# Kernel tuning notes

Measured on AMD Instinct MI355X. Metric: run time of the kernel, lower is better.

Reference implementation:

```python
import jax, jax.numpy as jnp
import numpy as np

N = 100000  # nodes

def gcn_layer(x, W, b, src, dst, norm):
    # x: [N, Fin] -> [N, Fout]; symmetric-normalized aggregation (PyG GCNConv)
    h = x @ W                                   # linear first (no bias yet)
    msg = h[src] * norm[:, None]                # gather + edge-wise scale
    out = jax.ops.segment_sum(msg, dst, num_segments=N)  # scatter-add to targets
    return out + b

def _prep_edges(edge_index):
    # add self loops
    loops = jnp.arange(N, dtype=edge_index.dtype)
    src = jnp.concatenate([edge_index[0], loops])
    dst = jnp.concatenate([edge_index[1], loops])
    # deg computed on target nodes with unit edge weights
    deg = jax.ops.segment_sum(jnp.ones_like(dst, dtype=jnp.float32), dst, num_segments=N)
    dinv = jnp.where(deg > 0, jax.lax.rsqrt(deg), 0.0)
    norm = dinv[src] * dinv[dst]
    return src, dst, norm

def setup_inputs() -> dict:
    key = jax.random.key(0)
    ks = jax.random.split(key, 8)
    F_in, H1, H2, C = 512, 256, 64, 10
    E = 3200000
    x = jax.random.normal(ks[0], (N, F_in), dtype=jnp.float32)
    edge_index = jax.random.randint(ks[1], (2, E), 0, N, dtype=jnp.int64)
    def glorot(k, fan_in, fan_out):
        s = jnp.sqrt(6.0 / (fan_in + fan_out))
        return jax.random.uniform(k, (fan_in, fan_out), jnp.float32, -s, s)
    return {
        "x": x,
        "edge_index": edge_index,
        "W1": glorot(ks[2], F_in, H1), "b1": jnp.zeros((H1,), jnp.float32),
        "W2": glorot(ks[3], H1, H2),   "b2": jnp.zeros((H2,), jnp.float32),
        "W3": glorot(ks[4], H2, C),    "b3": jnp.zeros((C,), jnp.float32),
    }

def reference(x, edge_index, W1, b1, W2, b2, W3, b3):
    src, dst, norm = _prep_edges(edge_index)
    h = jax.nn.relu(gcn_layer(x, W1, b1, src, dst, norm))
    h = jax.nn.relu(gcn_layer(h, W2, b2, src, dst, norm))
    h = gcn_layer(h, W3, b3, src, dst, norm)
    return jax.nn.log_softmax(h, axis=1)
```

## Files before the change

kernel.cpp:

```cpp
#include <hip/hip_runtime.h>
#include <math.h>

#define NNODES 100000
#define NEDGES 3200000
#define NB 391
#define PB 512
#define CHUNK 6250

typedef __attribute__((ext_vector_type(4))) float f32x4;
typedef __attribute__((ext_vector_type(2))) float f32x2;
typedef __attribute__((ext_vector_type(8))) short bf16x8;

__device__ __forceinline__ float bf2f(ushort u) {
    union { unsigned u; float f; } v; v.u = ((unsigned)u) << 16; return v.f;
}
__device__ __forceinline__ ushort f2bf(float f) {
    union { float f; unsigned u; } v; v.f = f;
    unsigned r = v.u + 0x7FFFu + ((v.u >> 16) & 1u);
    return (ushort)(r >> 16);
}

#if __has_builtin(__builtin_amdgcn_cvt_pk_fp8_f32) && __has_builtin(__builtin_amdgcn_cvt_pk_f32_fp8)
#define FP8_HW 1
#else
#define FP8_HW 0
#endif

__device__ __forceinline__ unsigned fp8enc_sw(float f) {
    union { float f; unsigned u; } v; v.f = f;
    unsigned sign = v.u >> 31;
    float a = fabsf(f);
    if (a >= 448.0f) return (sign << 7) | 0x7E;
    if (a < 0.0009765625f) return sign << 7;
    unsigned u = v.u & 0x7FFFFFFFu;
    u += 0x7FFFFu + ((u >> 20) & 1u);
    int e2 = (int)(u >> 23) - 127;
    if (e2 < -6) {
        int m = (int)(a * 512.0f + 0.5f); if (m > 7) m = 7;
        return (sign << 7) | (unsigned)m;
    }
    if (e2 > 8) return (sign << 7) | 0x7E;
    unsigned mant = (u >> 20) & 7u;
    return (sign << 7) | ((unsigned)(e2 + 7) << 3) | mant;
}
__device__ __forceinline__ float fp8dec_sw(unsigned b) {
    unsigned s = b >> 7, e = (b >> 3) & 0xF, m = b & 7;
    float v;
    if (e == 0) v = (float)m * 0.001953125f;
    else { union { unsigned u; float f; } x; x.u = ((e + 120u) << 23) | (m << 20); v = x.f; }
    return s ? -v : v;
}

__device__ __forceinline__ unsigned char f2fp8(float f) {
#if FP8_HW
    return (unsigned char)(__builtin_amdgcn_cvt_pk_fp8_f32(f, 0.f, 0, false) & 0xFF);
#else
    return (unsigned char)fp8enc_sw(f);
#endif
}
__device__ __forceinline__ void fp8x4_acc(unsigned w, float& ax, float& ay, float& az, float& aw) {
#if FP8_HW
    f32x2 lo = __builtin_amdgcn_cvt_pk_f32_fp8((int)w, false);
    f32x2 hi = __builtin_amdgcn_cvt_pk_f32_fp8((int)w, true);
    ax += lo[0]; ay += lo[1]; az += hi[0]; aw += hi[1];
#else
    ax += fp8dec_sw(w & 0xFF); ay += fp8dec_sw((w >> 8) & 0xFF);
    az += fp8dec_sw((w >> 16) & 0xFF); aw += fp8dec_sw(w >> 24);
#endif
}

__global__ void bucket_hist(const int* __restrict__ dst, int e, int* __restrict__ hist) {
    __shared__ int h[NB];
    const int b = blockIdx.x, t = threadIdx.x;
    for (int j = t; j < NB; j += 256) h[j] = 0;
    __syncthreads();
    const int lo = b * CHUNK;
    int hi = lo + CHUNK; if (hi > e) hi = e;
    for (int i = lo + t; i < hi; i += 256)
        atomicAdd(&h[dst[i] >> 8], 1);
    __syncthreads();
    for (int j = t; j < NB; j += 256) hist[b * NB + j] = h[j];
}

__global__ void scan_buckets(int* __restrict__ hist, int* __restrict__ btotal) {
    __shared__ int s[256];
    const int j = blockIdx.x, t = threadIdx.x;
    int v0 = hist[(2 * t) * NB + j];
    int v1 = hist[(2 * t + 1) * NB + j];
    int p = v0 + v1;
    s[t] = p;
    __syncthreads();
    for (int off = 1; off < 256; off <<= 1) {
        int u = (t >= off) ? s[t - off] : 0;
        __syncthreads();
        s[t] += u;
        __syncthreads();
    }
    int excl = s[t] - p;
    hist[(2 * t) * NB + j] = excl;
    hist[(2 * t + 1) * NB + j] = excl + v0;
    if (t == 255) btotal[j] = s[255];
}

__global__ void scan_btotal(const int* __restrict__ btotal, int* __restrict__ bstart, int e) {
    __shared__ int s[512];
    const int t = threadIdx.x;
    int v = (t < NB) ? btotal[t] : 0;
    s[t] = v;
    __syncthreads();
    for (int off = 1; off < 512; off <<= 1) {
        int u = (t >= off) ? s[t - off] : 0;
        __syncthreads();
        s[t] += u;
        __syncthreads();
    }
    if (t < NB) bstart[t] = s[t] - v;
    if (t == 0) bstart[NB] = e;
}

__global__ void bucket_scatter(const int* __restrict__ src, const int* __restrict__ dst, int e,
                               const int* __restrict__ hist, const int* __restrict__ bstart,
                               unsigned* __restrict__ bucketed) {
    __shared__ int off[NB];
    const int b = blockIdx.x, t = threadIdx.x;
    for (int j = t; j < NB; j += 256) off[j] = bstart[j] + hist[b * NB + j];
    __syncthreads();
    const int lo = b * CHUNK;
    int hi = lo + CHUNK; if (hi > e) hi = e;
    for (int i = lo + t; i < hi; i += 256) {
        int d = dst[i];
        int j = d >> 8;
        int p = atomicAdd(&off[j], 1);
        bucketed[p] = (unsigned)src[i] | ((unsigned)(d & 255) << 24);
    }
}

__global__ void bucket_finalize(const unsigned* __restrict__ bucketed, const int* __restrict__ bstart,
                                float* __restrict__ dinv, int* __restrict__ rowptr,
                                int* __restrict__ esrc, int n, int e) {
    __shared__ int h[256];
    __shared__ int s[256];
    __shared__ int rp[256];
    const int j = blockIdx.x, t = threadIdx.x;
    h[t] = 0;
    __syncthreads();
    const int lo = bstart[j], hi = bstart[j + 1];
    for (int i = lo + t; i < hi; i += 256)
        atomicAdd(&h[bucketed[i] >> 24], 1);
    __syncthreads();
    const int c = h[t] + 1;
    s[t] = c;
    __syncthreads();
    for (int off = 1; off < 256; off <<= 1) {
        int u = (t >= off) ? s[t - off] : 0;
        __syncthreads();
        s[t] += u;
        __syncthreads();
    }
    const int excl = s[t] - c;
    const int base = j << 8;
    const int node = base + t;
    const int myrp = bstart[j] + base + excl;
    rp[t] = myrp;
    if (node < n) {
        dinv[node] = rsqrtf((float)c);
        rowptr[node] = myrp;
        esrc[myrp] = node;
    }
    if (j == 0 && t == 0) rowptr[n] = e + n;
    h[t] = 0;
    __syncthreads();
    for (int i = lo + t; i < hi; i += 256) {
        unsigned ed = bucketed[i];
        int l = ed >> 24;
        int off = atomicAdd(&h[l], 1);
        esrc[rp[l] + 1 + off] = (int)(ed & 0xFFFFFFu);
    }
}

__global__ void conv_bf16(const float* __restrict__ x, ushort* __restrict__ xb, long n4) {
    long i = (long)blockIdx.x * blockDim.x + threadIdx.x;
    long stride = (long)gridDim.x * blockDim.x;
    for (; i < n4; i += stride) {
        float4 v = ((const float4*)x)[i];
        ushort4 o;
        o.x = f2bf(v.x); o.y = f2bf(v.y); o.z = f2bf(v.z); o.w = f2bf(v.w);
        ((ushort4*)xb)[i] = o;
    }
}

__global__ void conv_wt(const float* __restrict__ W, ushort* __restrict__ Wt,
                        int K, int N, int Npad) {
    int idx = blockIdx.x * blockDim.x + threadIdx.x;
    if (idx >= Npad * K) return;
    int n = idx / K, k = idx % K;
    Wt[idx] = (n < N) ? f2bf(W[(size_t)k * N + n]) : (ushort)0;
}

template <int BM, int BN, int BK, int WM, int WN, int OUTK>
__launch_bounds__(WM* WN * 64)
__global__ void gemm_bf16(const ushort* __restrict__ A, const ushort* __restrict__ Bt,
                          const float* __restrict__ dinv, void* __restrict__ Cout,
                          int M, int N, int K) {
    constexpr int NT = WM * WN * 64;
    __shared__ __align__(16) ushort As[BM][BK];
    __shared__ __align__(16) ushort Bs[BN][BK];
    const int tid = threadIdx.x;
    const int wid = tid >> 6, lane = tid & 63;
    const int wr = wid / WN, wc = wid % WN;
    constexpr int TM = BM / WM, TN = BN / WN;
    constexpr int FM = TM / 16, FN = TN / 16;
    const int m0 = blockIdx.y * BM, n0 = blockIdx.x * BN;
    const int ln = lane & 15, ks = (lane >> 4) * 8;

    f32x4 acc[FM][FN] = {};

    constexpr int ACH = BM * BK / 8;
    constexpr int BCH = BN * BK / 8;
    constexpr int CPR = BK / 8;

    for (int k0 = 0; k0 < K; k0 += BK) {
        #pragma unroll
        for (int it = 0; it < (ACH + NT - 1) / NT; ++it) {
            int c = it * NT + tid;
            if ((ACH % NT == 0) || (c < ACH)) {
                int row = c / CPR, ch = c % CPR;
                int gm = m0 + row; if (gm >= M) gm = M - 1;
                const ushort* gp = &A[(size_t)gm * K + k0 + ch * 8];
                __builtin_amdgcn_global_load_lds(
                    (const __attribute__((address_space(1))) void*)gp,
                    (__attribute__((address_space(3))) void*)((char*)&As[0][0] + c * 16),
                    16, 0, 0);
            }
        }
        #pragma unroll
        for (int it = 0; it < (BCH + NT - 1) / NT; ++it) {
            int c = it * NT + tid;
            if ((BCH % NT == 0) || (c < BCH)) {
                int row = c / CPR, ch = c % CPR;
                const ushort* gp = &Bt[(size_t)(n0 + row) * K + k0 + ch * 8];
                __builtin_amdgcn_global_load_lds(
                    (const __attribute__((address_space(1))) void*)gp,
                    (__attribute__((address_space(3))) void*)((char*)&Bs[0][0] + c * 16),
                    16, 0, 0);
            }
        }
        __syncthreads();

        bf16x8 af[FM], bfr[FN];
        #pragma unroll
        for (int mi = 0; mi < FM; ++mi)
            af[mi] = *(const bf16x8*)&As[wr * TM + mi * 16 + ln][ks];
        #pragma unroll
        for (int nj = 0; nj < FN; ++nj)
            bfr[nj] = *(const bf16x8*)&Bs[wc * TN + nj * 16 + ln][ks];
        #pragma unroll
        for (int mi = 0; mi < FM; ++mi)
            #pragma unroll
            for (int nj = 0; nj < FN; ++nj)
                acc[mi][nj] = __builtin_amdgcn_mfma_f32_16x16x32_bf16(af[mi], bfr[nj], acc[mi][nj], 0, 0, 0);
        __syncthreads();
    }

    const int rbase = (lane >> 4) * 4;
    #pragma unroll
    for (int mi = 0; mi < FM; ++mi) {
        #pragma unroll
        for (int r = 0; r < 4; ++r) {
            int gm = m0 + wr * TM + mi * 16 + rbase + r;
            if (gm >= M) continue;
            float d = dinv[gm];
            #pragma unroll
            for (int nj = 0; nj < FN; ++nj) {
                int gn = n0 + wc * TN + nj * 16 + ln;
                float v = acc[mi][nj][r] * d;
                if (OUTK == 1)      ((float*)Cout)[(size_t)gm * N + gn] = v;
                else if (OUTK == 0) ((ushort*)Cout)[(size_t)gm * N + gn] = f2bf(v);
                else                ((unsigned char*)Cout)[(size_t)gm * N + gn] = f2fp8(v);
            }
        }
    }
}

__global__ void agg1_fp8(const unsigned* __restrict__ h, const int* __restrict__ rowptr,
                         const int* __restrict__ esrc, const float* __restrict__ dinv,
                         const float* __restrict__ bias, ushort* __restrict__ out, int n) {
    const int wid = threadIdx.x >> 6, lane = threadIdx.x & 63;
    const int i = blockIdx.x * 4 + wid;
    if (i >= n) return;
    const int lo = rowptr[i], hi = rowptr[i + 1];
    float ax = 0.f, ay = 0.f, az = 0.f, aw = 0.f;
    int e = lo;
    for (; e + 7 < hi; e += 8) {
        int s[8];
        unsigned w[8];
        #pragma unroll
        for (int q = 0; q < 8; ++q) s[q] = esrc[e + q];
        #pragma unroll
        for (int q = 0; q < 8; ++q) w[q] = h[(size_t)s[q] * 64 + lane];
        #pragma unroll
        for (int q = 0; q < 8; ++q) fp8x4_acc(w[q], ax, ay, az, aw);
    }
    for (; e < hi; ++e)
        fp8x4_acc(h[(size_t)esrc[e] * 64 + lane], ax, ay, az, aw);

    float d = dinv[i];
    const int f0 = lane * 4;
    float4 b = *(const float4*)&bias[f0];
    ushort4 o;
    o.x = f2bf(fmaxf(ax * d + b.x, 0.f));
    o.y = f2bf(fmaxf(ay * d + b.y, 0.f));
    o.z = f2bf(fmaxf(az * d + b.z, 0.f));
    o.w = f2bf(fmaxf(aw * d + b.w, 0.f));
    *(ushort4*)&out[(size_t)i * 256 + f0] = o;
}

__global__ void agg2_fp8(const unsigned* __restrict__ h, const int* __restrict__ rowptr,
                         const int* __restrict__ esrc, const float* __restrict__ dinv,
                         const float* __restrict__ bias, ushort* __restrict__ out, int n) {
    const int g = threadIdx.x >> 4, j = threadIdx.x & 15;
    const int i = blockIdx.x * 16 + g;
    if (i >= n) return;
    const int lo = rowptr[i], hi = rowptr[i + 1];
    float ax = 0.f, ay = 0.f, az = 0.f, aw = 0.f;
    int e = lo;
    for (; e + 3 < hi; e += 4) {
        int s0 = esrc[e], s1 = esrc[e + 1], s2 = esrc[e + 2], s3 = esrc[e + 3];
        unsigned w0 = h[(size_t)s0 * 16 + j];
        unsigned w1 = h[(size_t)s1 * 16 + j];
        unsigned w2 = h[(size_t)s2 * 16 + j];
        unsigned w3 = h[(size_t)s3 * 16 + j];
        fp8x4_acc(w0, ax, ay, az, aw);
        fp8x4_acc(w1, ax, ay, az, aw);
        fp8x4_acc(w2, ax, ay, az, aw);
        fp8x4_acc(w3, ax, ay, az, aw);
    }
    for (; e < hi; ++e)
        fp8x4_acc(h[(size_t)esrc[e] * 16 + j], ax, ay, az, aw);

    float d = dinv[i];
    const int f0 = j * 4;
    float4 b = *(const float4*)&bias[f0];
    ushort4 o;
    o.x = f2bf(fmaxf(ax * d + b.x, 0.f));
    o.y = f2bf(fmaxf(ay * d + b.y, 0.f));
    o.z = f2bf(fmaxf(az * d + b.z, 0.f));
    o.w = f2bf(fmaxf(aw * d + b.w, 0.f));
    *(ushort4*)&out[(size_t)i * 64 + f0] = o;
}

__global__ void agg3_logsoftmax(const ushort* __restrict__ h3, const int* __restrict__ rowptr,
                                const int* __restrict__ esrc, const float* __restrict__ dinv,
                                const float* __restrict__ bias, float* __restrict__ out, int n) {
    const int g = threadIdx.x >> 3, j = threadIdx.x & 7;
    const int i = blockIdx.x * 32 + g;
    if (i >= n) return;
    const int lo = rowptr[i], hi = rowptr[i + 1];
    float a0 = 0.f, a1 = 0.f;
    int e = lo;
    for (; e + 3 < hi; e += 4) {
        int s0 = esrc[e], s1 = esrc[e + 1], s2 = esrc[e + 2], s3 = esrc[e + 3];
        unsigned w0 = *(const unsigned*)&h3[(size_t)s0 * 16 + 2 * j];
        unsigned w1 = *(const unsigned*)&h3[(size_t)s1 * 16 + 2 * j];
        unsigned w2 = *(const unsigned*)&h3[(size_t)s2 * 16 + 2 * j];
        unsigned w3 = *(const unsigned*)&h3[(size_t)s3 * 16 + 2 * j];
        a0 += bf2f((ushort)(w0 & 0xFFFF)) + bf2f((ushort)(w1 & 0xFFFF))
            + bf2f((ushort)(w2 & 0xFFFF)) + bf2f((ushort)(w3 & 0xFFFF));
        a1 += bf2f((ushort)(w0 >> 16)) + bf2f((ushort)(w1 >> 16))
            + bf2f((ushort)(w2 >> 16)) + bf2f((ushort)(w3 >> 16));
    }
    for (; e < hi; ++e) {
        unsigned w = *(const unsigned*)&h3[(size_t)esrc[e] * 16 + 2 * j];
        a0 += bf2f((ushort)(w & 0xFFFF));
        a1 += bf2f((ushort)(w >> 16));
    }
    const int f0 = 2 * j;
    float d = dinv[i];
    float v0 = (f0 < 10) ? (a0 * d + bias[f0]) : -INFINITY;
    float v1 = (f0 + 1 < 10) ? (a1 * d + bias[f0 + 1]) : -INFINITY;
    float m = fmaxf(v0, v1);
    #pragma unroll
    for (int off = 1; off < 8; off <<= 1) m = fmaxf(m, __shfl_xor(m, off, 8));
    float ex = ((f0 < 10) ? expf(v0 - m) : 0.f) + ((f0 + 1 < 10) ? expf(v1 - m) : 0.f);
    #pragma unroll
    for (int off = 1; off < 8; off <<= 1) ex += __shfl_xor(ex, off, 8);
    float ls = logf(ex);
    if (f0 < 10)     out[(size_t)i * 10 + f0] = v0 - m - ls;
    if (f0 + 1 < 10) out[(size_t)i * 10 + f0 + 1] = v1 - m - ls;
}

extern "C" void kernel_launch(void* const* d_in, const int* in_sizes, int n_in,
                              void* d_out, int out_size, void* d_ws, size_t ws_size,
                              hipStream_t stream) {
    const int N = NNODES, E = NEDGES;
    const float* x  = (const float*)d_in[0];
    const int*   ei = (const int*)d_in[1];
    const float* W1 = (const float*)d_in[2];
    const float* b1 = (const float*)d_in[3];
    const float* W2 = (const float*)d_in[4];
    const float* b2 = (const float*)d_in[5];
    const float* W3 = (const float*)d_in[6];
    const float* b3 = (const float*)d_in[7];
    float* out = (float*)d_out;
    const int* src = ei;
    const int* dst = ei + E;

    char* ws = (char*)d_ws;
    size_t off = 0;
    auto alloc = [&](size_t bytes) -> void* {
        void* p = ws + off;
        off = (off + bytes + 255) & ~(size_t)255;
        return p;
    };
    float* dinv   = (float*)alloc((size_t)N * 4);
    int*   rowptr = (int*)alloc((size_t)(N + 1) * 4);
    int*   btotal = (int*)alloc((size_t)NB * 4);
    int*   bstart = (int*)alloc((size_t)(NB + 1) * 4);
    int*   esrc   = (int*)alloc((size_t)(E + N) * 4);
    ushort* xb    = (ushort*)alloc((size_t)N * 512 * 2);
    ushort* W1t   = (ushort*)alloc((size_t)256 * 512 * 2);
    ushort* W2t   = (ushort*)alloc((size_t)64 * 256 * 2);
    ushort* W3t   = (ushort*)alloc((size_t)16 * 64 * 2);
    ushort* buf1  = (ushort*)alloc((size_t)N * 256 * 2);
    ushort* buf2  = (ushort*)alloc((size_t)N * 256 * 2);
    int*   hist   = (int*)buf1;
    unsigned* bucketed = (unsigned*)buf2;
    unsigned char* h1fp8 = (unsigned char*)buf1;
    unsigned char* h2fp8 = (unsigned char*)buf1;
    ushort* h3b   = (ushort*)xb;

    const int T = 256;
    bucket_hist<<<PB, T, 0, stream>>>(dst, E, hist);
    scan_buckets<<<NB, T, 0, stream>>>(hist, btotal);
    scan_btotal<<<1, 512, 0, stream>>>(btotal, bstart, E);
    bucket_scatter<<<PB, T, 0, stream>>>(src, dst, E, hist, bstart, bucketed);
    bucket_finalize<<<NB, T, 0, stream>>>(bucketed, bstart, dinv, rowptr, esrc, N, E);

    conv_bf16<<<2048, T, 0, stream>>>(x, xb, (long)N * 512 / 4);
    conv_wt<<<(256 * 512 + T - 1) / T, T, 0, stream>>>(W1, W1t, 512, 256, 256);
    conv_wt<<<(64 * 256 + T - 1) / T, T, 0, stream>>>(W2, W2t, 256, 64, 64);
    conv_wt<<<(16 * 64 + T - 1) / T, T, 0, stream>>>(W3, W3t, 64, 10, 16);

    const int MB = (N + 127) / 128;

    gemm_bf16<128, 128, 32, 2, 2, 2><<<dim3(2, MB), 256, 0, stream>>>(xb, W1t, dinv, h1fp8, N, 256, 512);
    agg1_fp8<<<(N + 3) / 4, 256, 0, stream>>>((const unsigned*)h1fp8, rowptr, esrc, dinv, b1, buf2, N);

    gemm_bf16<128, 64, 32, 2, 2, 2><<<dim3(1, MB), 256, 0, stream>>>(buf2, W2t, dinv, h2fp8, N, 64, 256);
    agg2_fp8<<<(N + 15) / 16, 256, 0, stream>>>((const unsigned*)h2fp8, rowptr, esrc, dinv, b2, buf2, N);

    gemm_bf16<128, 16, 32, 4, 1, 0><<<dim3(1, MB), 256, 0, stream>>>(buf2, W3t, dinv, h3b, N, 16, 64);
    agg3_logsoftmax<<<(N + 31) / 32, 256, 0, stream>>>(h3b, rowptr, esrc, dinv, b3, out, N);
}
```

Measured before the change: 429.2 us.

## Fuse fp32-to-bf16 conversion of x into first GEMM with full-N tile

Removes the separate conv_bf16 pass over x (read 200MB fp32, write 100MB bf16). The first-layer GEMM now reads fp32 x directly into LDS with async global-to-LDS loads and an XOR swizzle, then truncates to bf16 while building MFMA fragments. The tile widens to cover all 256 output columns so x is read only once. The cost is doubled A-tile LDS traffic, truncation instead of round-to-nearest, and a larger 512-thread block with more accumulators per wave.

```diff
diff --git a/kernel.cpp b/kernel.cpp
--- a/kernel.cpp
+++ b/kernel.cpp
@@ -18,6 +18,15 @@
     union { float f; unsigned u; } v; v.f = f;
     unsigned r = v.u + 0x7FFFu + ((v.u >> 16) & 1u);
     return (ushort)(r >> 16);
+}
+
+__device__ __forceinline__ unsigned pack_bf2(float f0, float f1) {
+    union { float f; unsigned u; } a, b; a.f = f0; b.f = f1;
+#if __has_builtin(__builtin_amdgcn_perm)
+    return __builtin_amdgcn_perm(b.u, a.u, 0x07060302u);
+#else
+    return (b.u & 0xFFFF0000u) | (a.u >> 16);
+#endif
 }
 
 #if __has_builtin(__builtin_amdgcn_cvt_pk_fp8_f32) && __has_builtin(__builtin_amdgcn_cvt_pk_f32_fp8)
@@ -178,23 +187,103 @@
     }
 }
 
-__global__ void conv_bf16(const float* __restrict__ x, ushort* __restrict__ xb, long n4) {
-    long i = (long)blockIdx.x * blockDim.x + threadIdx.x;
-    long stride = (long)gridDim.x * blockDim.x;
-    for (; i < n4; i += stride) {
-        float4 v = ((const float4*)x)[i];
-        ushort4 o;
-        o.x = f2bf(v.x); o.y = f2bf(v.y); o.z = f2bf(v.z); o.w = f2bf(v.w);
-        ((ushort4*)xb)[i] = o;
-    }
-}
-
 __global__ void conv_wt(const float* __restrict__ W, ushort* __restrict__ Wt,
                         int K, int N, int Npad) {
     int idx = blockIdx.x * blockDim.x + threadIdx.x;
     if (idx >= Npad * K) return;
     int n = idx / K, k = idx % K;
     Wt[idx] = (n < N) ? f2bf(W[(size_t)k * N + n]) : (ushort)0;
+}
+
+template <int BM, int BN, int BK, int WM, int WN>
+__launch_bounds__(WM* WN * 64)
+__global__ void gemm_f32a(const float* __restrict__ A, const ushort* __restrict__ Bt,
+                          const float* __restrict__ dinv, unsigned char* __restrict__ Cout,
+                          int M, int N, int K) {
+    constexpr int NT = WM * WN * 64;
+    __shared__ __align__(16) float Asf[BM][BK];
+    __shared__ __align__(16) ushort Bs[BN][BK];
+    const int tid = threadIdx.x;
+    const int wid = tid >> 6, lane = tid & 63;
+    const int wr = wid / WN, wc = wid % WN;
+    constexpr int TM = BM / WM, TN = BN / WN;
+    constexpr int FM = TM / 16, FN = TN / 16;
+    const int m0 = blockIdx.y * BM, n0 = blockIdx.x * BN;
+    const int ln = lane & 15, ks4 = (lane >> 4) * 2;
+
+    f32x4 acc[FM][FN] = {};
+
+    constexpr int CPRA = BK / 4;
+    constexpr int ACH = BM * CPRA;
+    constexpr int CPRB = BK / 8;
+    constexpr int BCH = BN * CPRB;
+
+    for (int k0 = 0; k0 < K; k0 += BK) {
+        #pragma unroll
+        for (int it = 0; it < ACH / NT; ++it) {
+            int c = it * NT + tid;
+            int row = c >> 3, chs = c & 7;
+            int gch = chs ^ (row & 7);
+            int gm = m0 + row; if (gm >= M) gm = M - 1;
+            const float* gp = &A[(size_t)gm * K + k0 + gch * 4];
+            __builtin_amdgcn_global_load_lds(
+                (const __attribute__((address_space(1))) void*)gp,
+                (__attribute__((address_space(3))) void*)((char*)&Asf[0][0] + c * 16),
+                16, 0, 0);
+        }
+        #pragma unroll
+        for (int it = 0; it < BCH / NT; ++it) {
+            int c = it * NT + tid;
+            int row = c / CPRB, ch = c % CPRB;
+            const ushort* gp = &Bt[(size_t)(n0 + row) * K + k0 + ch * 8];
+            __builtin_amdgcn_global_load_lds(
+                (const __attribute__((address_space(1))) void*)gp,
+                (__attribute__((address_space(3))) void*)((char*)&Bs[0][0] + c * 16),
+                16, 0, 0);
+        }
+        __syncthreads();
+
+        bf16x8 af[FM], bfr[FN];
+        #pragma unroll
+        for (int mi = 0; mi < FM; ++mi) {
+            int r = wr * TM + mi * 16 + ln;
+            const char* rowp = (const char*)&Asf[0][0] + r * (BK * 4);
+            float4 a0 = *(const float4*)(rowp + ((ks4 ^ (r & 7)) * 16));
+            float4 a1 = *(const float4*)(rowp + (((ks4 + 1) ^ (r & 7)) * 16));
+            union { unsigned w[4]; bf16x8 v; } u;
+            u.w[0] = pack_bf2(a0.x, a0.y);
+            u.w[1] = pack_bf2(a0.z, a0.w);
+            u.w[2] = pack_bf2(a1.x, a1.y);
+            u.w[3] = pack_bf2(a1.z, a1.w);
+            af[mi] = u.v;
+        }
+        const int ks = (lane >> 4) * 8;
+        #pragma unroll
+        for (int nj = 0; nj < FN; ++nj)
+            bfr[nj] = *(const bf16x8*)&Bs[wc * TN + nj * 16 + ln][ks];
+        #pragma unroll
+        for (int mi = 0; mi < FM; ++mi)
+            #pragma unroll
+            for (int nj = 0; nj < FN; ++nj)
+                acc[mi][nj] = __builtin_amdgcn_mfma_f32_16x16x32_bf16(af[mi], bfr[nj], acc[mi][nj], 0, 0, 0);
+        __syncthreads();
+    }
+
+    const int rbase = (lane >> 4) * 4;
+    #pragma unroll
+    for (int mi = 0; mi < FM; ++mi) {
+        #pragma unroll
+        for (int r = 0; r < 4; ++r) {
+            int gm = m0 + wr * TM + mi * 16 + rbase + r;
+            if (gm >= M) continue;
+            float d = dinv[gm];
+            #pragma unroll
+            for (int nj = 0; nj < FN; ++nj) {
+                int gn = n0 + wc * TN + nj * 16 + ln;
+                Cout[(size_t)gm * N + gn] = f2fp8(acc[mi][nj][r] * d);
+            }
+        }
+    }
 }
 
 template <int BM, int BN, int BK, int WM, int WN, int OUTK>
@@ -417,17 +506,16 @@
     int*   btotal = (int*)alloc((size_t)NB * 4);
     int*   bstart = (int*)alloc((size_t)(NB + 1) * 4);
     int*   esrc   = (int*)alloc((size_t)(E + N) * 4);
-    ushort* xb    = (ushort*)alloc((size_t)N * 512 * 2);
     ushort* W1t   = (ushort*)alloc((size_t)256 * 512 * 2);
     ushort* W2t   = (ushort*)alloc((size_t)64 * 256 * 2);
     ushort* W3t   = (ushort*)alloc((size_t)16 * 64 * 2);
+    ushort* h3b   = (ushort*)alloc((size_t)N * 16 * 2);
     ushort* buf1  = (ushort*)alloc((size_t)N * 256 * 2);
     ushort* buf2  = (ushort*)alloc((size_t)N * 256 * 2);
     int*   hist   = (int*)buf1;
     unsigned* bucketed = (unsigned*)buf2;
     unsigned char* h1fp8 = (unsigned char*)buf1;
     unsigned char* h2fp8 = (unsigned char*)buf1;
-    ushort* h3b   = (ushort*)xb;
 
     const int T = 256;
     bucket_hist<<<PB, T, 0, stream>>>(dst, E, hist);
@@ -436,14 +524,13 @@
     bucket_scatter<<<PB, T, 0, stream>>>(src, dst, E, hist, bstart, bucketed);
     bucket_finalize<<<NB, T, 0, stream>>>(bucketed, bstart, dinv, rowptr, esrc, N, E);
 
-    conv_bf16<<<2048, T, 0, stream>>>(x, xb, (long)N * 512 / 4);
     conv_wt<<<(256 * 512 + T - 1) / T, T, 0, stream>>>(W1, W1t, 512, 256, 256);
     conv_wt<<<(64 * 256 + T - 1) / T, T, 0, stream>>>(W2, W2t, 256, 64, 64);
     conv_wt<<<(16 * 64 + T - 1) / T, T, 0, stream>>>(W3, W3t, 64, 10, 16);
 
     const int MB = (N + 127) / 128;
 
-    gemm_bf16<128, 128, 32, 2, 2, 2><<<dim3(2, MB), 256, 0, stream>>>(xb, W1t, dinv, h1fp8, N, 256, 512);
+    gemm_f32a<128, 256, 32, 2, 4><<<dim3(1, MB), 512, 0, stream>>>(x, W1t, dinv, h1fp8, N, 256, 512);
     agg1_fp8<<<(N + 3) / 4, 256, 0, stream>>>((const unsigned*)h1fp8, rowptr, esrc, dinv, b1, buf2, N);
 
     gemm_bf16<128, 64, 32, 2, 2, 2><<<dim3(1, MB), 256, 0, stream>>>(buf2, W2t, dinv, h2fp8, N, 64, 256);
```

New measurement: 390.4 us. 1.1x faster.
